# Kernel tuning notes

Measured on AMD Instinct MI355X. Metric: run time of the kernel, lower is better.

The kernel has to match this reference:

```python
import jax, jax.numpy as jnp
import numpy as np

N, F, H, E, G, C = 100000, 128, 128, 640000, 512, 6
EPS = 1e-5


def setup_inputs() -> dict:
    key = jax.random.key(0)
    ks = jax.random.split(key, 20)
    def w(k, shape, fan_in):
        return jax.random.normal(k, shape, jnp.float32) * (1.0 / np.sqrt(fan_in))
    return {
        "x": jax.random.normal(ks[0], (N, F), jnp.float32),
        "edge_index": jax.random.randint(ks[1], (2, E), 0, N),
        "batch": jnp.sort(jax.random.randint(ks[2], (N,), 0, G)),
        "num_graphs": G,
        # SAGEConv1: lin_l (aggregated, with bias) + lin_r (root, no bias)
        "W1l": w(ks[3], (F, H), F), "b1l": jnp.zeros((H,), jnp.float32), "W1r": w(ks[4], (F, H), F),
        # SAGEConv2
        "W2l": w(ks[5], (H, H), H), "b2l": jnp.zeros((H,), jnp.float32), "W2r": w(ks[6], (H, H), H),
        # cluster heads
        "Wc1": w(ks[7], (H, H), H), "bc1": jnp.zeros((H,), jnp.float32),
        "Wc2": w(ks[8], (H, 2), H), "bc2": jnp.zeros((2,), jnp.float32),
        # classifier
        "Wl1": w(ks[9], (H, H), H), "bl1": jnp.zeros((H,), jnp.float32),
        "Wl2": w(ks[10], (H, C), H), "bl2": jnp.zeros((C,), jnp.float32),
    }


def _sage(x, src, dst, Wl, bl, Wr):
    # PyG SAGEConv: mean-aggregate messages x[src] at dst, then lin_l(agg) + lin_r(x)
    n = x.shape[0]
    s = jax.ops.segment_sum(x[src], dst, num_segments=n)
    cnt = jax.ops.segment_sum(jnp.ones((src.shape[0],), x.dtype), dst, num_segments=n)
    agg = s / jnp.maximum(cnt, 1.0)[:, None]
    return agg @ Wl + bl + x @ Wr


def reference(x, edge_index, batch, num_graphs,
              W1l, b1l, W1r, W2l, b2l, W2r,
              Wc1, bc1, Wc2, bc2, Wl1, bl1, Wl2, bl2):
    src, dst = edge_index[0], edge_index[1]
    h = jax.nn.relu(_sage(x, src, dst, W1l, b1l, W1r))
    h = jax.nn.relu(_sage(h, src, dst, W2l, b2l, W2r))
    # 2-way soft cluster assignment per node
    a = jax.nn.softmax(jnp.tanh(h @ Wc1 + bc1) @ Wc2 + bc2, axis=1)  # [N,2]
    g = num_graphs
    # group_features[g] = a_g^T h_g  -> per-node outer product, segment-summed by graph
    gf = jax.ops.segment_sum(a[:, :, None] * h[:, None, :], batch, num_segments=g)  # [G,2,H]
    pos = gf[:, 0, :]  # positive-cluster embedding per graph
    # new_adj[g] = a_g^T A_g a_g ; only within-graph edges appear in the per-graph adj block
    same = (batch[src] == batch[dst]).astype(h.dtype)
    contrib = same[:, None, None] * (a[src][:, :, None] * a[dst][:, None, :])  # [E,2,2]
    new_adj = jax.ops.segment_sum(contrib, batch[src], num_segments=g)  # [G,2,2]
    # F.normalize(p=1, dim=1, eps=1e-5): row-wise L1 with clamped denominator
    l1 = jnp.sum(jnp.abs(new_adj), axis=2, keepdims=True)
    norm_adj = new_adj / jnp.maximum(l1, EPS)
    diag = jnp.diagonal(norm_adj, axis1=1, axis2=2)  # [G,2]
    penalty = jnp.mean(jnp.mean((diag - 1.0) ** 2, axis=1))  # mse vs ones(2), averaged over graphs
    # NOTE: original (faithfully reproduced) takes the mean over ALL nodes, same for every graph
    graph_emb = jnp.broadcast_to(jnp.mean(h, axis=0, keepdims=True), (g, h.shape[1]))
    z = jax.nn.relu(pos @ Wl1 + bl1)  # dropout off (eval mode)
    logits = z @ Wl2 + bl2
    return (jax.nn.log_softmax(logits, axis=-1), pos, graph_emb, penalty)
```

## Files before the change

kernel.cpp:

```cpp
#include <hip/hip_runtime.h>

#define NN 100000
#define NE 640000
#define HD 128
#define NG 512
#define NC 6
#define EPSV 1e-5f

typedef __bf16 bf16_t;
typedef bf16_t bf16x8 __attribute__((ext_vector_type(8)));
typedef float f32x4 __attribute__((ext_vector_type(4)));
typedef unsigned short ushort_t;

__device__ __forceinline__ float b2f(unsigned int u16) {
    return __builtin_bit_cast(float, u16 << 16);
}
__device__ __forceinline__ unsigned short f2b(float f) {
    unsigned int u = __builtin_bit_cast(unsigned int, f);
    unsigned int r = (u + 0x7fffu + ((u >> 16) & 1u)) >> 16;
    return (unsigned short)r;
}

__global__ __launch_bounds__(256) void k_cvt(const float* __restrict__ in,
                                             unsigned short* __restrict__ out, int n8) {
    int i = blockIdx.x * 256 + threadIdx.x;
    if (i >= n8) return;
    float4 v0 = reinterpret_cast<const float4*>(in)[i * 2];
    float4 v1 = reinterpret_cast<const float4*>(in)[i * 2 + 1];
    unsigned short u[8] = {f2b(v0.x), f2b(v0.y), f2b(v0.z), f2b(v0.w),
                           f2b(v1.x), f2b(v1.y), f2b(v1.z), f2b(v1.w)};
    reinterpret_cast<uint4*>(out)[i] = *reinterpret_cast<uint4*>(u);
}

__global__ __launch_bounds__(256) void k_prepw(const float* __restrict__ W,
                                               unsigned short* __restrict__ Wt) {
    int i = blockIdx.x * 256 + threadIdx.x;
    int k = i >> 7, n = i & 127;
    Wt[n * HD + k] = f2b(W[k * HD + n]);
}

__global__ void k_count(const int* __restrict__ dst, int* __restrict__ cnt) {
    int e = blockIdx.x * blockDim.x + threadIdx.x;
    if (e < NE) atomicAdd(&cnt[dst[e]], 1);
}

__global__ void k_scan1(const int* __restrict__ cnt, int* __restrict__ excl,
                        int* __restrict__ bsum, int n) {
    __shared__ int sh[256];
    int i = blockIdx.x * 256 + threadIdx.x;
    int v = (i < n) ? cnt[i] : 0;
    sh[threadIdx.x] = v;
    __syncthreads();
    for (int off = 1; off < 256; off <<= 1) {
        int t = (threadIdx.x >= off) ? sh[threadIdx.x - off] : 0;
        __syncthreads();
        sh[threadIdx.x] += t;
        __syncthreads();
    }
    if (i < n) excl[i] = sh[threadIdx.x] - v;
    if (threadIdx.x == 255) bsum[blockIdx.x] = sh[255];
}

__global__ void k_scan2(int* bsum, int nb) {
    __shared__ int sh[512];
    int t = threadIdx.x;
    sh[t] = (t < nb) ? bsum[t] : 0;
    __syncthreads();
    for (int off = 1; off < 512; off <<= 1) {
        int v = (t >= off) ? sh[t - off] : 0;
        __syncthreads();
        sh[t] += v;
        __syncthreads();
    }
    if (t < nb) bsum[t] = sh[t];
}

__global__ void k_scan3(const int* __restrict__ excl, const int* __restrict__ bsum,
                        int* __restrict__ row_off, int n) {
    int i = blockIdx.x * 256 + threadIdx.x;
    if (i < n) row_off[i] = excl[i] + (blockIdx.x ? bsum[blockIdx.x - 1] : 0);
    if (i == 0) row_off[n] = NE;
}

__global__ void k_fill(const int* __restrict__ src, const int* __restrict__ dst,
                       const int* __restrict__ row_off, int* __restrict__ fillp,
                       int* __restrict__ csr) {
    int e = blockIdx.x * blockDim.x + threadIdx.x;
    if (e < NE) {
        int d = dst[e];
        int p = atomicAdd(&fillp[d], 1);
        csr[row_off[d] + p] = src[e];
    }
}

__global__ __launch_bounds__(256) void k_gather_b(const unsigned short* __restrict__ X,
                                                  const int* __restrict__ row_off,
                                                  const int* __restrict__ csr,
                                                  unsigned short* __restrict__ out) {
    int node = (blockIdx.x * blockDim.x + threadIdx.x) >> 6;
    int lane = threadIdx.x & 63;
    if (node >= NN) return;
    int beg = row_off[node], end = row_off[node + 1];
    int grp = lane >> 4;
    int sub = lane & 15;
    float acc[8] = {0.f, 0.f, 0.f, 0.f, 0.f, 0.f, 0.f, 0.f};
    for (int j = beg; j < end; j += 4) {
        int jj = j + grp;
        bool valid = jj < end;
        int s = csr[valid ? jj : beg];
        uint4 v = *reinterpret_cast<const uint4*>(X + (size_t)s * HD + sub * 8);
        if (valid) {
            acc[0] += b2f(v.x & 0xffffu); acc[1] += b2f(v.x >> 16);
            acc[2] += b2f(v.y & 0xffffu); acc[3] += b2f(v.y >> 16);
            acc[4] += b2f(v.z & 0xffffu); acc[5] += b2f(v.z >> 16);
            acc[6] += b2f(v.w & 0xffffu); acc[7] += b2f(v.w >> 16);
        }
    }
#pragma unroll
    for (int k = 0; k < 8; ++k) {
        acc[k] += __shfl_xor(acc[k], 16, 64);
        acc[k] += __shfl_xor(acc[k], 32, 64);
    }
    if (grp == 0) {
        float inv = 1.f / fmaxf((float)(end - beg), 1.f);
        unsigned short u[8];
#pragma unroll
        for (int k = 0; k < 8; ++k) u[k] = f2b(acc[k] * inv);
        *reinterpret_cast<uint4*>(out + (size_t)node * HD + sub * 8) = *reinterpret_cast<uint4*>(u);
    }
}

__global__ __launch_bounds__(256) void mfma_dual(
    const unsigned short* __restrict__ A1, const unsigned short* __restrict__ W1t,
    const unsigned short* __restrict__ A2, const unsigned short* __restrict__ W2t,
    const float* __restrict__ bias, unsigned short* __restrict__ out, int M)
{
    __shared__ uint4 wlds[2048];
    const int wid = threadIdx.x >> 6;
    const int lane = threadIdx.x & 63;
    const int lrow = lane & 15;
    const int lkg = lane >> 4;
    const int r0 = blockIdx.x * 128 + wid * 32;

    bf16x8 a[2][2][4];
#pragma unroll
    for (int s = 0; s < 2; ++s) {
        const unsigned short* Ap = s ? A2 : A1;
#pragma unroll
        for (int g = 0; g < 2; ++g) {
            int row = r0 + g * 16 + lrow;
            row = row < M ? row : M - 1;
            const unsigned short* p = Ap + (size_t)row * HD + lkg * 8;
#pragma unroll
            for (int ks = 0; ks < 4; ++ks)
                a[s][g][ks] = *reinterpret_cast<const bf16x8*>(p + ks * 32);
        }
    }

    f32x4 acc[2][8];
#pragma unroll
    for (int t = 0; t < 8; ++t) {
        float b = bias[t * 16 + lrow];
        acc[0][t] = (f32x4){b, b, b, b};
        acc[1][t] = (f32x4){b, b, b, b};
    }

    const char* ldsb = (const char*)wlds;
#pragma unroll
    for (int s = 0; s < 2; ++s) {
        const uint4* g4 = reinterpret_cast<const uint4*>(s ? W2t : W1t);
        if (s) __syncthreads();
        for (int i = threadIdx.x; i < 2048; i += 256) {
            int di = i ^ ((i >> 4) & 7);
            wlds[di] = g4[i];
        }
        __syncthreads();
#pragma unroll
        for (int ks = 0; ks < 4; ++ks) {
#pragma unroll
            for (int t = 0; t < 8; ++t) {
                int off = (lrow * 256 + lkg * 16 + t * 4096 + ks * 64) ^ ((lrow & 7) << 4);
                bf16x8 b = *reinterpret_cast<const bf16x8*>(ldsb + off);
                acc[0][t] = __builtin_amdgcn_mfma_f32_16x16x32_bf16(a[s][0][ks], b, acc[0][t], 0, 0, 0);
                acc[1][t] = __builtin_amdgcn_mfma_f32_16x16x32_bf16(a[s][1][ks], b, acc[1][t], 0, 0, 0);
            }
        }
    }

#pragma unroll
    for (int g = 0; g < 2; ++g)
#pragma unroll
        for (int t = 0; t < 8; ++t)
#pragma unroll
            for (int r = 0; r < 4; ++r) {
                int row = r0 + g * 16 + lkg * 4 + r;
                if (row < M) {
                    float v = fmaxf(acc[g][t][r], 0.f);
                    out[(size_t)row * HD + t * 16 + lrow] = f2b(v);
                }
            }
}

__global__ __launch_bounds__(256) void mfma_attn(
    const unsigned short* __restrict__ A1, const unsigned short* __restrict__ W1t,
    const float* __restrict__ bias, const float* __restrict__ Wc2,
    const float* __restrict__ bc2, float* __restrict__ a2, int M)
{
    __shared__ uint4 wlds[2048];
    const int wid = threadIdx.x >> 6;
    const int lane = threadIdx.x & 63;
    const int lrow = lane & 15;
    const int lkg = lane >> 4;
    const int r0 = blockIdx.x * 128 + wid * 32;

    bf16x8 a[2][4];
#pragma unroll
    for (int g = 0; g < 2; ++g) {
        int row = r0 + g * 16 + lrow;
        row = row < M ? row : M - 1;
        const unsigned short* p = A1 + (size_t)row * HD + lkg * 8;
#pragma unroll
        for (int ks = 0; ks < 4; ++ks)
            a[g][ks] = *reinterpret_cast<const bf16x8*>(p + ks * 32);
    }

    f32x4 acc[2][8];
#pragma unroll
    for (int t = 0; t < 8; ++t) {
        float b = bias[t * 16 + lrow];
        acc[0][t] = (f32x4){b, b, b, b};
        acc[1][t] = (f32x4){b, b, b, b};
    }

    const uint4* g4 = reinterpret_cast<const uint4*>(W1t);
    for (int i = threadIdx.x; i < 2048; i += 256) {
        int di = i ^ ((i >> 4) & 7);
        wlds[di] = g4[i];
    }
    __syncthreads();

    const char* ldsb = (const char*)wlds;
#pragma unroll
    for (int ks = 0; ks < 4; ++ks) {
#pragma unroll
        for (int t = 0; t < 8; ++t) {
            int off = (lrow * 256 + lkg * 16 + t * 4096 + ks * 64) ^ ((lrow & 7) << 4);
            bf16x8 b = *reinterpret_cast<const bf16x8*>(ldsb + off);
            acc[0][t] = __builtin_amdgcn_mfma_f32_16x16x32_bf16(a[0][ks], b, acc[0][t], 0, 0, 0);
            acc[1][t] = __builtin_amdgcn_mfma_f32_16x16x32_bf16(a[1][ks], b, acc[1][t], 0, 0, 0);
        }
    }

    float p0[2][4] = {{0.f, 0.f, 0.f, 0.f}, {0.f, 0.f, 0.f, 0.f}};
    float p1[2][4] = {{0.f, 0.f, 0.f, 0.f}, {0.f, 0.f, 0.f, 0.f}};
#pragma unroll
    for (int t = 0; t < 8; ++t) {
        float2 wv = reinterpret_cast<const float2*>(Wc2)[t * 16 + lrow];
#pragma unroll
        for (int g = 0; g < 2; ++g)
#pragma unroll
            for (int r = 0; r < 4; ++r) {
                float tv = tanhf(acc[g][t][r]);
                p0[g][r] = fmaf(tv, wv.x, p0[g][r]);
                p1[g][r] = fmaf(tv, wv.y, p1[g][r]);
            }
    }
#pragma unroll
    for (int off = 1; off < 16; off <<= 1) {
#pragma unroll
        for (int g = 0; g < 2; ++g)
#pragma unroll
            for (int r = 0; r < 4; ++r) {
                p0[g][r] += __shfl_xor(p0[g][r], off, 64);
                p1[g][r] += __shfl_xor(p1[g][r], off, 64);
            }
    }
    if (lrow == 0) {
        float B0 = bc2[0], B1 = bc2[1];
#pragma unroll
        for (int g = 0; g < 2; ++g)
#pragma unroll
            for (int r = 0; r < 4; ++r) {
                int row = r0 + g * 16 + lkg * 4 + r;
                if (row < M) {
                    float u0 = p0[g][r] + B0, u1 = p1[g][r] + B1;
                    float m = fmaxf(u0, u1);
                    float e0 = expf(u0 - m), e1 = expf(u1 - m);
                    float inv = 1.f / (e0 + e1);
                    reinterpret_cast<float2*>(a2)[row] = (float2){e0 * inv, e1 * inv};
                }
            }
    }
}

__global__ __launch_bounds__(512) void k_pos(const unsigned short* __restrict__ h,
                                             const float* __restrict__ a2,
                                             const int* __restrict__ batch,
                                             float* __restrict__ pos_out,
                                             float* __restrict__ csum) {
    __shared__ float4 sh[8][64];
    int g = blockIdx.x;
    int lo = 0, hi = NN;
    while (lo < hi) { int m = (lo + hi) >> 1; if (batch[m] < g) lo = m + 1; else hi = m; }
    int beg = lo;
    hi = NN;
    while (lo < hi) { int m = (lo + hi) >> 1; if (batch[m] < g + 1) lo = m + 1; else hi = m; }
    int end = lo;
    int grp = threadIdx.x >> 6;
    int lane = threadIdx.x & 63;
    float4 acc = {0.f, 0.f, 0.f, 0.f};
    for (int i = beg + grp; i < end; i += 8) {
        float a = a2[i * 2];
        unsigned int v = *reinterpret_cast<const unsigned int*>(h + (size_t)i * HD + lane * 2);
        float f0 = b2f(v & 0xffffu), f1 = b2f(v >> 16);
        acc.x = fmaf(a, f0, acc.x);
        acc.y = fmaf(a, f1, acc.y);
        acc.z += f0;
        acc.w += f1;
    }
    sh[grp][lane] = acc;
    __syncthreads();
    if (threadIdx.x < 64) {
        float4 s = sh[0][lane];
#pragma unroll
        for (int k = 1; k < 8; ++k) {
            float4 t = sh[k][lane];
            s.x += t.x; s.y += t.y; s.z += t.z; s.w += t.w;
        }
        reinterpret_cast<float2*>(pos_out)[g * 64 + lane] = (float2){s.x, s.y};
        atomicAdd(&csum[lane * 2], s.z);
        atomicAdd(&csum[lane * 2 + 1], s.w);
    }
}

__global__ void k_gemb(const float* __restrict__ csum, float* __restrict__ out) {
    int i = blockIdx.x * 256 + threadIdx.x;
    out[i] = csum[i & 127] * (1.f / (float)NN);
}

__global__ __launch_bounds__(256) void k_adj(const int* __restrict__ src, const int* __restrict__ dst,
                                             const int* __restrict__ batch, const float* __restrict__ a2,
                                             float* __restrict__ adj) {
    __shared__ float sh[NG * 4];
    for (int i = threadIdx.x; i < NG * 4; i += 256) sh[i] = 0.f;
    __syncthreads();
    for (int e = blockIdx.x * 256 + threadIdx.x; e < NE; e += gridDim.x * 256) {
        int s = src[e], d = dst[e];
        int bs = batch[s], bd = batch[d];
        if (bs != bd) continue;
        float a0s = a2[2 * s], a1s = a2[2 * s + 1];
        float a0d = a2[2 * d], a1d = a2[2 * d + 1];
        float* A = sh + bs * 4;
        atomicAdd(A + 0, a0s * a0d);
        atomicAdd(A + 1, a0s * a1d);
        atomicAdd(A + 2, a1s * a0d);
        atomicAdd(A + 3, a1s * a1d);
    }
    __syncthreads();
    for (int i = threadIdx.x; i < NG * 4; i += 256) {
        float v = sh[i];
        if (v != 0.f) atomicAdd(&adj[i], v);
    }
}

__global__ void k_penalty(const float* __restrict__ adj, float* __restrict__ out) {
    __shared__ float sh[512];
    int g = threadIdx.x;
    float x0 = adj[g * 4], x1 = adj[g * 4 + 1], x2 = adj[g * 4 + 2], x3 = adj[g * 4 + 3];
    float l0 = fabsf(x0) + fabsf(x1);
    float l1 = fabsf(x2) + fabsf(x3);
    float d0 = x0 / fmaxf(l0, EPSV);
    float d1 = x3 / fmaxf(l1, EPSV);
    sh[g] = 0.5f * ((d0 - 1.f) * (d0 - 1.f) + (d1 - 1.f) * (d1 - 1.f));
    __syncthreads();
    for (int off = 256; off >= 1; off >>= 1) {
        if (g < off) sh[g] += sh[g + off];
        __syncthreads();
    }
    if (g == 0) out[0] = sh[0] * (1.f / (float)NG);
}

__global__ __launch_bounds__(256) void gemm_head(
    const float* __restrict__ A, const float* __restrict__ W,
    const float* __restrict__ bias, float* __restrict__ out, int M)
{
    const int tid = threadIdx.x;
    const int w = __builtin_amdgcn_readfirstlane(tid >> 6);
    const int lane = tid & 63;
    const int r0 = blockIdx.x * 32 + w * 8;
    if (r0 >= M) return;
    const int c0 = lane, c1 = lane + 64;
    float acc0[8], acc1[8];
    const float b0 = bias[c0], b1 = bias[c1];
#pragma unroll
    for (int r = 0; r < 8; ++r) { acc0[r] = b0; acc1[r] = b1; }
    const float* Ap = A + (size_t)r0 * HD;
    for (int k4 = 0; k4 < HD / 4; ++k4) {
        float4 a[8];
#pragma unroll
        for (int r = 0; r < 8; ++r)
            a[r] = *reinterpret_cast<const float4*>(Ap + r * HD + k4 * 4);
#pragma unroll
        for (int j = 0; j < 4; ++j) {
            const int k = k4 * 4 + j;
            const float w0 = W[k * HD + c0];
            const float w1 = W[k * HD + c1];
#pragma unroll
            for (int r = 0; r < 8; ++r) {
                const float av = (j == 0) ? a[r].x : (j == 1) ? a[r].y
                               : (j == 2) ? a[r].z : a[r].w;
                acc0[r] = fmaf(av, w0, acc0[r]);
                acc1[r] = fmaf(av, w1, acc1[r]);
            }
        }
    }
#pragma unroll
    for (int r = 0; r < 8; ++r) {
        out[(size_t)(r0 + r) * HD + c0] = fmaxf(acc0[r], 0.f);
        out[(size_t)(r0 + r) * HD + c1] = fmaxf(acc1[r], 0.f);
    }
}

__global__ void k_head(const float* __restrict__ z, const float* __restrict__ Wl2,
                       const float* __restrict__ bl2, float* __restrict__ out0) {
    int g = blockIdx.x * blockDim.x + threadIdx.x;
    if (g >= NG) return;
    float l[NC];
#pragma unroll
    for (int c = 0; c < NC; ++c) l[c] = bl2[c];
    for (int k = 0; k < HD; ++k) {
        float zv = z[(size_t)g * HD + k];
#pragma unroll
        for (int c = 0; c < NC; ++c) l[c] = fmaf(zv, Wl2[k * NC + c], l[c]);
    }
    float m = l[0];
#pragma unroll
    for (int c = 1; c < NC; ++c) m = fmaxf(m, l[c]);
    float sum = 0.f;
#pragma unroll
    for (int c = 0; c < NC; ++c) sum += expf(l[c] - m);
    float lse = m + logf(sum);
#pragma unroll
    for (int c = 0; c < NC; ++c) out0[g * NC + c] = l[c] - lse;
}

extern "C" void kernel_launch(void* const* d_in, const int* in_sizes, int n_in,
                              void* d_out, int out_size, void* d_ws, size_t ws_size,
                              hipStream_t stream) {
    const float* x   = (const float*)d_in[0];
    const int*   ei  = (const int*)d_in[1];
    const int*   src = ei;
    const int*   dst = ei + NE;
    const int*   batch = (const int*)d_in[2];
    const float* W1l = (const float*)d_in[4];
    const float* b1l = (const float*)d_in[5];
    const float* W1r = (const float*)d_in[6];
    const float* W2l = (const float*)d_in[7];
    const float* b2l = (const float*)d_in[8];
    const float* W2r = (const float*)d_in[9];
    const float* Wc1 = (const float*)d_in[10];
    const float* bc1 = (const float*)d_in[11];
    const float* Wc2 = (const float*)d_in[12];
    const float* bc2 = (const float*)d_in[13];
    const float* Wl1 = (const float*)d_in[14];
    const float* bl1 = (const float*)d_in[15];
    const float* Wl2 = (const float*)d_in[16];
    const float* bl2 = (const float*)d_in[17];

    char* ws = (char*)d_ws;
    const size_t BB = (size_t)NN * HD * 2;
    unsigned short* xb   = (unsigned short*)(ws);
    unsigned short* bufA = (unsigned short*)(ws + BB);
    unsigned short* bufB = (unsigned short*)(ws + 2 * BB);
    size_t O = 3 * BB;
    int*   cnt     = (int*)(ws + O);
    int*   excl    = (int*)(ws + O + 400000);
    int*   row_off = (int*)(ws + O + 800000);
    int*   fillp   = (int*)(ws + O + 1200064);
    int*   csr     = (int*)(ws + O + 1600064);
    int*   bsum    = (int*)(ws + O + 4160064);
    float* a2      = (float*)(ws + O + 4164160);
    float* adj     = (float*)(ws + O + 4964160);
    float* csum    = (float*)(ws + O + 4972352);
    float* zbuf    = (float*)(ws + O + 4972864);
    unsigned short* w1lt = (unsigned short*)(ws + O + 5235008);
    unsigned short* w1rt = w1lt + 16384;
    unsigned short* w2lt = w1rt + 16384;
    unsigned short* w2rt = w2lt + 16384;
    unsigned short* wc1t = w2rt + 16384;

    float* out0 = (float*)d_out;
    float* pos  = out0 + NG * NC;
    float* gemb = pos + NG * HD;
    float* pen  = gemb + NG * HD;

    hipMemsetAsync(cnt, 0, NN * 4, stream);
    hipMemsetAsync(fillp, 0, NN * 4, stream);
    hipMemsetAsync(adj, 0, NG * 4 * 4, stream);
    hipMemsetAsync(csum, 0, HD * 4, stream);

    k_cvt<<<6250, 256, 0, stream>>>(x, xb, NN * HD / 8);
    k_prepw<<<64, 256, 0, stream>>>(W1l, w1lt);
    k_prepw<<<64, 256, 0, stream>>>(W1r, w1rt);
    k_prepw<<<64, 256, 0, stream>>>(W2l, w2lt);
    k_prepw<<<64, 256, 0, stream>>>(W2r, w2rt);
    k_prepw<<<64, 256, 0, stream>>>(Wc1, wc1t);

    k_count<<<NE / 256, 256, 0, stream>>>(dst, cnt);
    k_scan1<<<391, 256, 0, stream>>>(cnt, excl, bsum, NN);
    k_scan2<<<1, 512, 0, stream>>>(bsum, 391);
    k_scan3<<<391, 256, 0, stream>>>(excl, bsum, row_off, NN);
    k_fill<<<NE / 256, 256, 0, stream>>>(src, dst, row_off, fillp, csr);

    const int GEMM_GRID = (NN + 127) / 128;
    k_gather_b<<<NN / 4, 256, 0, stream>>>(xb, row_off, csr, bufA);
    mfma_dual<<<GEMM_GRID, 256, 0, stream>>>(bufA, w1lt, xb, w1rt, b1l, bufB, NN);
    k_gather_b<<<NN / 4, 256, 0, stream>>>(bufB, row_off, csr, bufA);
    mfma_dual<<<GEMM_GRID, 256, 0, stream>>>(bufA, w2lt, bufB, w2rt, b2l, xb, NN);
    mfma_attn<<<GEMM_GRID, 256, 0, stream>>>(xb, wc1t, bc1, Wc2, bc2, a2, NN);
    k_pos<<<NG, 512, 0, stream>>>(xb, a2, batch, pos, csum);
    k_gemb<<<NG * HD / 256, 256, 0, stream>>>(csum, gemb);
    k_adj<<<120, 256, 0, stream>>>(src, dst, batch, a2, adj);
    k_penalty<<<1, 512, 0, stream>>>(adj, pen);
    gemm_head<<<NG / 32, 256, 0, stream>>>(pos, Wl1, bl1, zbuf, NG);
    k_head<<<2, 256, 0, stream>>>(zbuf, Wl2, bl2, out0);
}
```

Before: 336.6 us.

## Merge weight prep launches, reuse count buffer in CSR fill, unroll gather

Combines the five weight transpose/convert launches into one kernel and the four memsets into one contiguous memset. The CSR fill now counts down from the per-node count array instead of using a separate zeroed fill counter, and it writes with nontemporal stores. The neighbor gather processes eight edges per iteration with two accumulators to raise memory-level parallelism. Filling in reverse order changes the within-row order of neighbors, and with it the floating-point summation order.

```diff
diff --git a/kernel.cpp b/kernel.cpp
--- a/kernel.cpp
+++ b/kernel.cpp
@@ -10,7 +10,6 @@
 typedef __bf16 bf16_t;
 typedef bf16_t bf16x8 __attribute__((ext_vector_type(8)));
 typedef float f32x4 __attribute__((ext_vector_type(4)));
-typedef unsigned short ushort_t;
 
 __device__ __forceinline__ float b2f(unsigned int u16) {
     return __builtin_bit_cast(float, u16 << 16);
@@ -32,11 +31,15 @@
     reinterpret_cast<uint4*>(out)[i] = *reinterpret_cast<uint4*>(u);
 }
 
-__global__ __launch_bounds__(256) void k_prepw(const float* __restrict__ W,
-                                               unsigned short* __restrict__ Wt) {
+__global__ __launch_bounds__(256) void k_prepw_all(
+    const float* __restrict__ Wa, const float* __restrict__ Wb,
+    const float* __restrict__ Wc, const float* __restrict__ Wd,
+    const float* __restrict__ We, unsigned short* __restrict__ Wt) {
     int i = blockIdx.x * 256 + threadIdx.x;
-    int k = i >> 7, n = i & 127;
-    Wt[n * HD + k] = f2b(W[k * HD + n]);
+    int w = i >> 14, r = i & 16383;
+    int k = r >> 7, n = r & 127;
+    const float* W = (w == 0) ? Wa : (w == 1) ? Wb : (w == 2) ? Wc : (w == 3) ? Wd : We;
+    Wt[w * 16384 + n * HD + k] = f2b(W[k * HD + n]);
 }
 
 __global__ void k_count(const int* __restrict__ dst, int* __restrict__ cnt) {
@@ -83,13 +86,13 @@
 }
 
 __global__ void k_fill(const int* __restrict__ src, const int* __restrict__ dst,
-                       const int* __restrict__ row_off, int* __restrict__ fillp,
+                       const int* __restrict__ row_off, int* __restrict__ cnt,
                        int* __restrict__ csr) {
     int e = blockIdx.x * blockDim.x + threadIdx.x;
     if (e < NE) {
         int d = dst[e];
-        int p = atomicAdd(&fillp[d], 1);
-        csr[row_off[d] + p] = src[e];
+        int p = atomicSub(&cnt[d], 1);
+        __builtin_nontemporal_store(src[e], &csr[row_off[d] + p - 1]);
     }
 }
 
@@ -103,29 +106,40 @@
     int beg = row_off[node], end = row_off[node + 1];
     int grp = lane >> 4;
     int sub = lane & 15;
-    float acc[8] = {0.f, 0.f, 0.f, 0.f, 0.f, 0.f, 0.f, 0.f};
-    for (int j = beg; j < end; j += 4) {
-        int jj = j + grp;
-        bool valid = jj < end;
-        int s = csr[valid ? jj : beg];
-        uint4 v = *reinterpret_cast<const uint4*>(X + (size_t)s * HD + sub * 8);
-        if (valid) {
-            acc[0] += b2f(v.x & 0xffffu); acc[1] += b2f(v.x >> 16);
-            acc[2] += b2f(v.y & 0xffffu); acc[3] += b2f(v.y >> 16);
-            acc[4] += b2f(v.z & 0xffffu); acc[5] += b2f(v.z >> 16);
-            acc[6] += b2f(v.w & 0xffffu); acc[7] += b2f(v.w >> 16);
+    float accA[8] = {0.f, 0.f, 0.f, 0.f, 0.f, 0.f, 0.f, 0.f};
+    float accB[8] = {0.f, 0.f, 0.f, 0.f, 0.f, 0.f, 0.f, 0.f};
+    for (int j = beg; j < end; j += 8) {
+        int jj0 = j + grp, jj1 = j + 4 + grp;
+        bool ok0 = jj0 < end, ok1 = jj1 < end;
+        int s0 = csr[ok0 ? jj0 : beg];
+        int s1 = csr[ok1 ? jj1 : beg];
+        uint4 v0 = *reinterpret_cast<const uint4*>(X + (size_t)s0 * HD + sub * 8);
+        uint4 v1 = *reinterpret_cast<const uint4*>(X + (size_t)s1 * HD + sub * 8);
+        if (ok0) {
+            accA[0] += b2f(v0.x & 0xffffu); accA[1] += b2f(v0.x >> 16);
+            accA[2] += b2f(v0.y & 0xffffu); accA[3] += b2f(v0.y >> 16);
+            accA[4] += b2f(v0.z & 0xffffu); accA[5] += b2f(v0.z >> 16);
+            accA[6] += b2f(v0.w & 0xffffu); accA[7] += b2f(v0.w >> 16);
+        }
+        if (ok1) {
+            accB[0] += b2f(v1.x & 0xffffu); accB[1] += b2f(v1.x >> 16);
+            accB[2] += b2f(v1.y & 0xffffu); accB[3] += b2f(v1.y >> 16);
+            accB[4] += b2f(v1.z & 0xffffu); accB[5] += b2f(v1.z >> 16);
+            accB[6] += b2f(v1.w & 0xffffu); accB[7] += b2f(v1.w >> 16);
         }
     }
 #pragma unroll
     for (int k = 0; k < 8; ++k) {
-        acc[k] += __shfl_xor(acc[k], 16, 64);
-        acc[k] += __shfl_xor(acc[k], 32, 64);
+        float a = accA[k] + accB[k];
+        a += __shfl_xor(a, 16, 64);
+        a += __shfl_xor(a, 32, 64);
+        accA[k] = a;
     }
     if (grp == 0) {
         float inv = 1.f / fmaxf((float)(end - beg), 1.f);
         unsigned short u[8];
 #pragma unroll
-        for (int k = 0; k < 8; ++k) u[k] = f2b(acc[k] * inv);
+        for (int k = 0; k < 8; ++k) u[k] = f2b(accA[k] * inv);
         *reinterpret_cast<uint4*>(out + (size_t)node * HD + sub * 8) = *reinterpret_cast<uint4*>(u);
     }
 }
@@ -474,16 +488,15 @@
     unsigned short* bufB = (unsigned short*)(ws + 2 * BB);
     size_t O = 3 * BB;
     int*   cnt     = (int*)(ws + O);
-    int*   excl    = (int*)(ws + O + 400000);
-    int*   row_off = (int*)(ws + O + 800000);
-    int*   fillp   = (int*)(ws + O + 1200064);
-    int*   csr     = (int*)(ws + O + 1600064);
-    int*   bsum    = (int*)(ws + O + 4160064);
-    float* a2      = (float*)(ws + O + 4164160);
-    float* adj     = (float*)(ws + O + 4964160);
-    float* csum    = (float*)(ws + O + 4972352);
-    float* zbuf    = (float*)(ws + O + 4972864);
-    unsigned short* w1lt = (unsigned short*)(ws + O + 5235008);
+    float* adj     = (float*)(ws + O + 400000);
+    float* csum    = (float*)(ws + O + 408192);
+    int*   excl    = (int*)(ws + O + 408704);
+    int*   row_off = (int*)(ws + O + 808704);
+    int*   csr     = (int*)(ws + O + 1208768);
+    int*   bsum    = (int*)(ws + O + 3768768);
+    float* a2      = (float*)(ws + O + 3772864);
+    float* zbuf    = (float*)(ws + O + 4572864);
+    unsigned short* w1lt = (unsigned short*)(ws + O + 4835008);
     unsigned short* w1rt = w1lt + 16384;
     unsigned short* w2lt = w1rt + 16384;
     unsigned short* w2rt = w2lt + 16384;
@@ -494,23 +507,16 @@
     float* gemb = pos + NG * HD;
     float* pen  = gemb + NG * HD;
 
-    hipMemsetAsync(cnt, 0, NN * 4, stream);
-    hipMemsetAsync(fillp, 0, NN * 4, stream);
-    hipMemsetAsync(adj, 0, NG * 4 * 4, stream);
-    hipMemsetAsync(csum, 0, HD * 4, stream);
+    hipMemsetAsync(ws + O, 0, 408704, stream);
 
     k_cvt<<<6250, 256, 0, stream>>>(x, xb, NN * HD / 8);
-    k_prepw<<<64, 256, 0, stream>>>(W1l, w1lt);
-    k_prepw<<<64, 256, 0, stream>>>(W1r, w1rt);
-    k_prepw<<<64, 256, 0, stream>>>(W2l, w2lt);
-    k_prepw<<<64, 256, 0, stream>>>(W2r, w2rt);
-    k_prepw<<<64, 256, 0, stream>>>(Wc1, wc1t);
+    k_prepw_all<<<320, 256, 0, stream>>>(W1l, W1r, W2l, W2r, Wc1, w1lt);
 
     k_count<<<NE / 256, 256, 0, stream>>>(dst, cnt);
     k_scan1<<<391, 256, 0, stream>>>(cnt, excl, bsum, NN);
     k_scan2<<<1, 512, 0, stream>>>(bsum, 391);
     k_scan3<<<391, 256, 0, stream>>>(excl, bsum, row_off, NN);
-    k_fill<<<NE / 256, 256, 0, stream>>>(src, dst, row_off, fillp, csr);
+    k_fill<<<NE / 256, 256, 0, stream>>>(src, dst, row_off, cnt, csr);
 
     const int GEMM_GRID = (NN + 127) / 128;
     k_gather_b<<<NN / 4, 256, 0, stream>>>(xb, row_off, csr, bufA);
```

Result: no change. 336.4 us (-0.1%).
